# Kernel tuning notes

Hardware: AMD Instinct MI355X
Metric: run time of the kernel (lower is better)

## Reference

```python
import jax, jax.numpy as jnp
import numpy as np


def _lstm_cell(x_t, h, c, w_ih, w_hh, b):
    # x_t, h, c: [B, 1]; w_ih, w_hh: [4, 1]; b: [4]
    # PyTorch gate order: input, forget, cell(g), output
    gates = x_t @ w_ih.T + h @ w_hh.T + b  # [B, 4]
    i, f, g, o = jnp.split(gates, 4, axis=-1)
    i = jax.nn.sigmoid(i)
    f = jax.nn.sigmoid(f)
    o = jax.nn.sigmoid(o)
    g = jnp.tanh(g)
    c = f * c + i * g
    h = o * jnp.tanh(c)
    return h, c


def setup_inputs() -> dict:
    key = jax.random.key(0)
    ks = jax.random.split(key, 8)
    B, T_IN, STEPS = 32768, 1024, 512
    return {
        "x": jax.random.normal(ks[0], (B, 1, T_IN), dtype=jnp.float32),
        "t": jax.random.normal(ks[1], (B, 1, STEPS), dtype=jnp.float32),
        "h0": jax.random.normal(ks[2], (B, 1), dtype=jnp.float32),
        "c0": jax.random.normal(ks[3], (B, 1), dtype=jnp.float32),
        "w_ih": jax.random.normal(ks[4], (4, 1), dtype=jnp.float32),
        "w_hh": jax.random.normal(ks[5], (4, 1), dtype=jnp.float32),
        "b_ih": jax.random.normal(ks[6], (4,), dtype=jnp.float32) * 0.1,
        "b_hh": jax.random.normal(ks[7], (4,), dtype=jnp.float32) * 0.1,
    }


def reference(x, t, h0, c0, w_ih, w_hh, b_ih, b_hh):
    b = b_ih + b_hh
    # open loop: feed every input timestep through the LSTM cell
    xs = jnp.transpose(x[:, 0, :], (1, 0))[:, :, None]  # [T_in, B, 1]

    def open_step(carry, x_t):
        h, c = carry
        h, c = _lstm_cell(x_t, h, c, w_ih, w_hh, b)
        return (h, c), None

    (h, c), _ = jax.lax.scan(open_step, (h0, c0), xs)

    ts = jnp.transpose(t[:, 0, :], (1, 0))[:, :, None]  # [steps, B, 1]

    def closed_step(carry, _):
        h, c, x_in = carry
        h, c = _lstm_cell(x_in, h, c, w_ih, w_hh, b)
        return (h, c, h), h

    steps = ts.shape[0]
    _, preds = jax.lax.scan(closed_step, (h, c, xs[-1]), None, length=steps)
    # criterion = MSELoss(mean), accumulated per step:
    # sum_t mean_B((pred_t - t_t)^2)
    loss = jnp.sum(jnp.mean((preds - ts) ** 2, axis=(1, 2)))
    # pred_seq is detached numpy in the original -> stop_gradient here
    pred_seq = jax.lax.stop_gradient(jnp.transpose(preds[:, :, 0], (1, 0)))  # [B, steps]
    return loss, pred_seq
```

## Files before the change

### kernel.cpp

```cpp
#include <hip/hip_runtime.h>


#define L2E 1.44269504088896340736f
#define B_TOT 32768
#define T_IN 1024
#define STEPS 512
#define CH 64
#define PAD 65

__device__ __forceinline__ float ex2(float x){ return __builtin_amdgcn_exp2f(x); }
__device__ __forceinline__ float rcp(float x){ return __builtin_amdgcn_rcpf(x); }

struct K8 { float Ai,Bi,Ci, Af,Bf,Cf, Ag,Bg,Cg, Ao,Bo,Co; };
struct K4 { float Wi,Ci, Wf,Cf, Wg,Cg, Wo,Co; };

__device__ __forceinline__ void step_open(float xv, float& h, float& c, const K8& K){
    float zi = fmaf(h, K.Bi, fmaf(xv, K.Ai, K.Ci));
    float zf = fmaf(h, K.Bf, fmaf(xv, K.Af, K.Cf));
    float zg = fmaf(h, K.Bg, fmaf(xv, K.Ag, K.Cg));
    float zo = fmaf(h, K.Bo, fmaf(xv, K.Ao, K.Co));
    float ri = rcp(1.0f + ex2(zi));
    float rf = rcp(1.0f + ex2(zf));
    float rg = rcp(1.0f + ex2(zg));
    float ro = rcp(1.0f + ex2(zo));
    float g  = fmaf(-2.0f, rg, 1.0f);
    c = fmaf(rf, c, ri * g);
    float rc = rcp(1.0f + ex2((2.0f * L2E) * c));
    h = ro * fmaf(-2.0f, rc, 1.0f);
}

__device__ __forceinline__ void step_closed(float& h, float& c, const K4& K){
    float zi = fmaf(h, K.Wi, K.Ci);
    float zf = fmaf(h, K.Wf, K.Cf);
    float zg = fmaf(h, K.Wg, K.Cg);
    float zo = fmaf(h, K.Wo, K.Co);
    float ri = rcp(1.0f + ex2(zi));
    float rf = rcp(1.0f + ex2(zf));
    float rg = rcp(1.0f + ex2(zg));
    float ro = rcp(1.0f + ex2(zo));
    float g  = fmaf(-2.0f, rg, 1.0f);
    c = fmaf(rf, c, ri * g);
    float rc = rcp(1.0f + ex2((2.0f * L2E) * c));
    h = ro * fmaf(-2.0f, rc, 1.0f);
}

__device__ __forceinline__ void stage_issue(const float* __restrict__ base,
                                            int row_stride, int col0, int lane,
                                            float4* v){
    const int r_lo = lane >> 4;
    const int c4   = lane & 15;
    #pragma unroll
    for (int j = 0; j < 16; ++j){
        int r = j * 4 + r_lo;
        v[j] = *(const float4*)(base + (size_t)r * row_stride + col0 + c4 * 4);
    }
}
__device__ __forceinline__ void stage_write(float* __restrict__ lds, int lane,
                                            const float4* v){
    const int r_lo = lane >> 4;
    const int c4   = lane & 15;
    #pragma unroll
    for (int j = 0; j < 16; ++j){
        int r = j * 4 + r_lo;
        float* p = lds + r * PAD + c4 * 4;
        p[0] = v[j].x; p[1] = v[j].y; p[2] = v[j].z; p[3] = v[j].w;
    }
}

__global__ __launch_bounds__(64) void lstm_chain_kernel(
    const float* __restrict__ x, const float* __restrict__ t,
    const float* __restrict__ h0, const float* __restrict__ c0,
    const float* __restrict__ w_ih, const float* __restrict__ w_hh,
    const float* __restrict__ b_ih, const float* __restrict__ b_hh,
    float* __restrict__ out)
{
    __shared__ float sb[2][64 * PAD];
    __shared__ float pb[64 * PAD];

    const int lane = threadIdx.x;
    const int b0 = blockIdx.x * 64;
    const int b = b0 + lane;

    K8 K; K4 K2;
    {
        float bi = b_ih[0] + b_hh[0], bf = b_ih[1] + b_hh[1];
        float bg = b_ih[2] + b_hh[2], bo = b_ih[3] + b_hh[3];
        K.Ai = -L2E * w_ih[0]; K.Bi = -L2E * w_hh[0]; K.Ci = -L2E * bi;
        K.Af = -L2E * w_ih[1]; K.Bf = -L2E * w_hh[1]; K.Cf = -L2E * bf;
        K.Ag =  2.0f * L2E * w_ih[2]; K.Bg = 2.0f * L2E * w_hh[2]; K.Cg = 2.0f * L2E * bg;
        K.Ao = -L2E * w_ih[3]; K.Bo = -L2E * w_hh[3]; K.Co = -L2E * bo;
        K2.Wi = K.Ai + K.Bi; K2.Ci = K.Ci;
        K2.Wf = K.Af + K.Bf; K2.Cf = K.Cf;
        K2.Wg = K.Ag + K.Bg; K2.Cg = K.Cg;
        K2.Wo = K.Ao + K.Bo; K2.Co = K.Co;
    }

    float h = h0[b];
    float c = c0[b];

    const float* xbase = x + (size_t)b0 * T_IN;
    const float* tbase = t + (size_t)b0 * STEPS;

    {
        float4 stg[16];
        stage_issue(xbase, T_IN, 0, lane, stg);
        stage_write(sb[0], lane, stg);
    }
    #pragma unroll 1
    for (int k = 0; k < T_IN / CH; ++k){
        float4 stg2[16];
        if (k < T_IN / CH - 1) stage_issue(xbase, T_IN, (k + 1) * CH, lane, stg2);
        const float* xrow = &sb[k & 1][lane * PAD];
        #pragma unroll 4
        for (int s = 0; s < CH; ++s){
            step_open(xrow[s], h, c, K);
        }
        if (k < T_IN / CH - 1) stage_write(sb[(k + 1) & 1], lane, stg2);
    }
    float xin = sb[(T_IN / CH - 1) & 1][lane * PAD + (CH - 1)];

    {
        float4 stg[16];
        stage_issue(tbase, STEPS, 0, lane, stg);
        stage_write(sb[0], lane, stg);
    }
    float lacc = 0.0f;
    #pragma unroll 1
    for (int k = 0; k < STEPS / CH; ++k){
        float4 stg2[16];
        if (k < STEPS / CH - 1) stage_issue(tbase, STEPS, (k + 1) * CH, lane, stg2);
        const float* trow = &sb[k & 1][lane * PAD];
        float* prow = &pb[lane * PAD];
        #pragma unroll 4
        for (int s = 0; s < CH; ++s){
            if (k == 0 && s == 0) step_open(xin, h, c, K);
            else                  step_closed(h, c, K2);
            float d = h - trow[s];
            lacc = fmaf(d, d, lacc);
            prow[s] = h;
        }
        float* obase = out + 1 + (size_t)b0 * STEPS + k * CH + lane;
        #pragma unroll 4
        for (int r = 0; r < 64; ++r){
            obase[(size_t)r * STEPS] = pb[r * PAD + lane];
        }
        if (k < STEPS / CH - 1) stage_write(sb[(k + 1) & 1], lane, stg2);
    }

    #pragma unroll
    for (int off = 32; off > 0; off >>= 1)
        lacc += __shfl_down(lacc, off, 64);
    if (lane == 0)
        atomicAdd(out, lacc * (1.0f / (float)B_TOT));
}

extern "C" void kernel_launch(void* const* d_in, const int* in_sizes, int n_in,
                              void* d_out, int out_size, void* d_ws, size_t ws_size,
                              hipStream_t stream) {
    const float* x    = (const float*)d_in[0];
    const float* t    = (const float*)d_in[1];
    const float* h0   = (const float*)d_in[2];
    const float* c0   = (const float*)d_in[3];
    const float* w_ih = (const float*)d_in[4];
    const float* w_hh = (const float*)d_in[5];
    const float* b_ih = (const float*)d_in[6];
    const float* b_hh = (const float*)d_in[7];
    float* out = (float*)d_out;

    hipMemsetAsync(out, 0, sizeof(float), stream);

    lstm_chain_kernel<<<B_TOT / 64, 64, 0, stream>>>(
        x, t, h0, c0, w_ih, w_hh, b_ih, b_hh, out);
}
```

Measured before the change: 355.4 us.

## Split each LSTM chain across two lanes with DPP gate exchange

Each batch element's recurrence is now handled by a lane pair: one lane computes input/cell gates, the other forget/output, exchanging sigmoid results via DPP quad permute. Blocks cover 32 chains instead of 64, doubling the wave count to fill more SIMDs and shortening the per-step transcendental chain per lane. The cell state is kept prescaled to fold a multiply, and the loss is halved to account for duplicated lanes. Costs include redundant cell/tanh work in both lanes and extra DPP/select instructions.

New measurement: 331.1 us. 6.8% less time.

```diff
diff --git a/kernel.cpp b/kernel.cpp
--- a/kernel.cpp
+++ b/kernel.cpp
@@ -5,65 +5,53 @@
 #define B_TOT 32768
 #define T_IN 1024
 #define STEPS 512
+#define CPB 32
 #define CH 64
 #define PAD 65
 
 __device__ __forceinline__ float ex2(float x){ return __builtin_amdgcn_exp2f(x); }
 __device__ __forceinline__ float rcp(float x){ return __builtin_amdgcn_rcpf(x); }
-
-struct K8 { float Ai,Bi,Ci, Af,Bf,Cf, Ag,Bg,Cg, Ao,Bo,Co; };
-struct K4 { float Wi,Ci, Wf,Cf, Wg,Cg, Wo,Co; };
-
-__device__ __forceinline__ void step_open(float xv, float& h, float& c, const K8& K){
-    float zi = fmaf(h, K.Bi, fmaf(xv, K.Ai, K.Ci));
-    float zf = fmaf(h, K.Bf, fmaf(xv, K.Af, K.Cf));
-    float zg = fmaf(h, K.Bg, fmaf(xv, K.Ag, K.Cg));
-    float zo = fmaf(h, K.Bo, fmaf(xv, K.Ao, K.Co));
-    float ri = rcp(1.0f + ex2(zi));
-    float rf = rcp(1.0f + ex2(zf));
-    float rg = rcp(1.0f + ex2(zg));
-    float ro = rcp(1.0f + ex2(zo));
-    float g  = fmaf(-2.0f, rg, 1.0f);
-    c = fmaf(rf, c, ri * g);
-    float rc = rcp(1.0f + ex2((2.0f * L2E) * c));
-    h = ro * fmaf(-2.0f, rc, 1.0f);
+__device__ __forceinline__ float dpp_swap1(float v){
+    return __int_as_float(__builtin_amdgcn_mov_dpp(__float_as_int(v), 0xB1, 0xF, 0xF, true));
 }
 
-__device__ __forceinline__ void step_closed(float& h, float& c, const K4& K){
-    float zi = fmaf(h, K.Wi, K.Ci);
-    float zf = fmaf(h, K.Wf, K.Cf);
-    float zg = fmaf(h, K.Wg, K.Cg);
-    float zo = fmaf(h, K.Wo, K.Co);
-    float ri = rcp(1.0f + ex2(zi));
-    float rf = rcp(1.0f + ex2(zf));
-    float rg = rcp(1.0f + ex2(zg));
-    float ro = rcp(1.0f + ex2(zo));
-    float g  = fmaf(-2.0f, rg, 1.0f);
-    c = fmaf(rf, c, ri * g);
-    float rc = rcp(1.0f + ex2((2.0f * L2E) * c));
-    h = ro * fmaf(-2.0f, rc, 1.0f);
+struct LaneK { float A1,B1,C1, A2,B2,C2, W1,W2; };
+
+__device__ __forceinline__ void finish_step(float z1, float z2, bool odd,
+                                            float& h, float& C){
+    float e1 = ex2(z1);
+    float e2 = ex2(z2);
+    float r1 = rcp(1.0f + e1);
+    float r2 = rcp(1.0f + e2);
+    float s1 = dpp_swap1(r1);
+    float s2 = dpp_swap1(r2);
+    float ri = odd ? s1 : r1;
+    float rf = odd ? r1 : s1;
+    float rg = odd ? s2 : r2;
+    float ro = odd ? r2 : s2;
+    float g2  = fmaf(rg, -4.0f * L2E, 2.0f * L2E);
+    float rfC = rf * C;
+    C = fmaf(ri, g2, rfC);
+    float rc = rcp(1.0f + ex2(C));
+    float u  = rc + rc;
+    h = fmaf(-u, ro, ro);
 }
 
-__device__ __forceinline__ void stage_issue(const float* __restrict__ base,
-                                            int row_stride, int col0, int lane,
-                                            float4* v){
-    const int r_lo = lane >> 4;
-    const int c4   = lane & 15;
+__device__ __forceinline__ void stage_issue32(const float* __restrict__ base,
+                                              int row_stride, int col0, int lane,
+                                              float4* v){
+    const int r_lo = lane >> 4, c4 = lane & 15;
     #pragma unroll
-    for (int j = 0; j < 16; ++j){
-        int r = j * 4 + r_lo;
-        v[j] = *(const float4*)(base + (size_t)r * row_stride + col0 + c4 * 4);
-    }
+    for (int j = 0; j < 8; ++j)
+        v[j] = *(const float4*)(base + (size_t)(j*4 + r_lo) * row_stride + col0 + c4*4);
 }
-__device__ __forceinline__ void stage_write(float* __restrict__ lds, int lane,
-                                            const float4* v){
-    const int r_lo = lane >> 4;
-    const int c4   = lane & 15;
+__device__ __forceinline__ void stage_write32(float* __restrict__ lds, int lane,
+                                              const float4* v){
+    const int r_lo = lane >> 4, c4 = lane & 15;
     #pragma unroll
-    for (int j = 0; j < 16; ++j){
-        int r = j * 4 + r_lo;
-        float* p = lds + r * PAD + c4 * 4;
-        p[0] = v[j].x; p[1] = v[j].y; p[2] = v[j].z; p[3] = v[j].w;
+    for (int j = 0; j < 8; ++j){
+        float* p = lds + (j*4 + r_lo) * PAD + c4*4;
+        p[0]=v[j].x; p[1]=v[j].y; p[2]=v[j].z; p[3]=v[j].w;
     }
 }
 
@@ -74,84 +62,93 @@
     const float* __restrict__ b_ih, const float* __restrict__ b_hh,
     float* __restrict__ out)
 {
-    __shared__ float sb[2][64 * PAD];
-    __shared__ float pb[64 * PAD];
+    __shared__ float sb[2][CPB * PAD];
+    __shared__ float pb[CPB * PAD];
 
     const int lane = threadIdx.x;
-    const int b0 = blockIdx.x * 64;
-    const int b = b0 + lane;
+    const bool odd = lane & 1;
+    const int ch   = lane >> 1;
+    const int b0   = blockIdx.x * CPB;
 
-    K8 K; K4 K2;
+    LaneK K;
     {
         float bi = b_ih[0] + b_hh[0], bf = b_ih[1] + b_hh[1];
         float bg = b_ih[2] + b_hh[2], bo = b_ih[3] + b_hh[3];
-        K.Ai = -L2E * w_ih[0]; K.Bi = -L2E * w_hh[0]; K.Ci = -L2E * bi;
-        K.Af = -L2E * w_ih[1]; K.Bf = -L2E * w_hh[1]; K.Cf = -L2E * bf;
-        K.Ag =  2.0f * L2E * w_ih[2]; K.Bg = 2.0f * L2E * w_hh[2]; K.Cg = 2.0f * L2E * bg;
-        K.Ao = -L2E * w_ih[3]; K.Bo = -L2E * w_hh[3]; K.Co = -L2E * bo;
-        K2.Wi = K.Ai + K.Bi; K2.Ci = K.Ci;
-        K2.Wf = K.Af + K.Bf; K2.Cf = K.Cf;
-        K2.Wg = K.Ag + K.Bg; K2.Cg = K.Cg;
-        K2.Wo = K.Ao + K.Bo; K2.Co = K.Co;
+        float Ai = -L2E*w_ih[0], Bi = -L2E*w_hh[0], Ci = -L2E*bi;
+        float Af = -L2E*w_ih[1], Bf = -L2E*w_hh[1], Cf = -L2E*bf;
+        float Ag = 2.0f*L2E*w_ih[2], Bg = 2.0f*L2E*w_hh[2], Cg = 2.0f*L2E*bg;
+        float Ao = -L2E*w_ih[3], Bo = -L2E*w_hh[3], Co = -L2E*bo;
+        K.A1 = odd ? Af : Ai;  K.B1 = odd ? Bf : Bi;  K.C1 = odd ? Cf : Ci;
+        K.A2 = odd ? Ao : Ag;  K.B2 = odd ? Bo : Bg;  K.C2 = odd ? Co : Cg;
+        K.W1 = K.A1 + K.B1;    K.W2 = K.A2 + K.B2;
     }
 
-    float h = h0[b];
-    float c = c0[b];
+    float h = h0[b0 + ch];
+    float C = (2.0f * L2E) * c0[b0 + ch];
 
     const float* xbase = x + (size_t)b0 * T_IN;
     const float* tbase = t + (size_t)b0 * STEPS;
 
-    {
-        float4 stg[16];
-        stage_issue(xbase, T_IN, 0, lane, stg);
-        stage_write(sb[0], lane, stg);
-    }
+    { float4 stg[8]; stage_issue32(xbase, T_IN, 0, lane, stg); stage_write32(sb[0], lane, stg); }
     #pragma unroll 1
     for (int k = 0; k < T_IN / CH; ++k){
-        float4 stg2[16];
-        if (k < T_IN / CH - 1) stage_issue(xbase, T_IN, (k + 1) * CH, lane, stg2);
-        const float* xrow = &sb[k & 1][lane * PAD];
+        float4 stg[8];
+        if (k < T_IN/CH - 1) stage_issue32(xbase, T_IN, (k+1)*CH, lane, stg);
+        const float* xrow = &sb[k & 1][ch * PAD];
         #pragma unroll 4
         for (int s = 0; s < CH; ++s){
-            step_open(xrow[s], h, c, K);
+            float xv = xrow[s];
+            float z1 = fmaf(xv, K.A1, fmaf(h, K.B1, K.C1));
+            float z2 = fmaf(xv, K.A2, fmaf(h, K.B2, K.C2));
+            finish_step(z1, z2, odd, h, C);
         }
-        if (k < T_IN / CH - 1) stage_write(sb[(k + 1) & 1], lane, stg2);
+        if (k < T_IN/CH - 1) stage_write32(sb[(k+1) & 1], lane, stg);
     }
-    float xin = sb[(T_IN / CH - 1) & 1][lane * PAD + (CH - 1)];
+    float xin = sb[(T_IN/CH - 1) & 1][ch * PAD + (CH - 1)];
 
-    {
-        float4 stg[16];
-        stage_issue(tbase, STEPS, 0, lane, stg);
-        stage_write(sb[0], lane, stg);
-    }
+    { float4 stg[8]; stage_issue32(tbase, STEPS, 0, lane, stg); stage_write32(sb[0], lane, stg); }
     float lacc = 0.0f;
+
+    auto cstep = [&](int s, const float* trow, float* prow){
+        float z1 = fmaf(h, K.W1, K.C1);
+        float z2 = fmaf(h, K.W2, K.C2);
+        finish_step(z1, z2, odd, h, C);
+        float d = h - trow[s];
+        lacc = fmaf(d, d, lacc);
+        prow[s] = h;
+    };
+
     #pragma unroll 1
     for (int k = 0; k < STEPS / CH; ++k){
-        float4 stg2[16];
-        if (k < STEPS / CH - 1) stage_issue(tbase, STEPS, (k + 1) * CH, lane, stg2);
-        const float* trow = &sb[k & 1][lane * PAD];
-        float* prow = &pb[lane * PAD];
+        float4 stg[8];
+        if (k < STEPS/CH - 1) stage_issue32(tbase, STEPS, (k+1)*CH, lane, stg);
+        const float* trow = &sb[k & 1][ch * PAD];
+        float* prow = &pb[ch * PAD];
+        if (k == 0){
+            float z1 = fmaf(xin, K.A1, fmaf(h, K.B1, K.C1));
+            float z2 = fmaf(xin, K.A2, fmaf(h, K.B2, K.C2));
+            finish_step(z1, z2, odd, h, C);
+            float d = h - trow[0];
+            lacc = fmaf(d, d, lacc);
+            prow[0] = h;
+            #pragma unroll 4
+            for (int s = 1; s < CH; ++s) cstep(s, trow, prow);
+        } else {
+            #pragma unroll 4
+            for (int s = 0; s < CH; ++s) cstep(s, trow, prow);
+        }
+        float* obase = out + 1 + (size_t)b0 * STEPS + k * CH;
         #pragma unroll 4
-        for (int s = 0; s < CH; ++s){
-            if (k == 0 && s == 0) step_open(xin, h, c, K);
-            else                  step_closed(h, c, K2);
-            float d = h - trow[s];
-            lacc = fmaf(d, d, lacc);
-            prow[s] = h;
-        }
-        float* obase = out + 1 + (size_t)b0 * STEPS + k * CH + lane;
-        #pragma unroll 4
-        for (int r = 0; r < 64; ++r){
-            obase[(size_t)r * STEPS] = pb[r * PAD + lane];
-        }
-        if (k < STEPS / CH - 1) stage_write(sb[(k + 1) & 1], lane, stg2);
+        for (int r = 0; r < CPB; ++r)
+            obase[(size_t)r * STEPS + lane] = pb[r * PAD + lane];
+        if (k < STEPS/CH - 1) stage_write32(sb[(k+1) & 1], lane, stg);
     }
 
     #pragma unroll
     for (int off = 32; off > 0; off >>= 1)
         lacc += __shfl_down(lacc, off, 64);
     if (lane == 0)
-        atomicAdd(out, lacc * (1.0f / (float)B_TOT));
+        atomicAdd(out, lacc * (0.5f / (float)B_TOT));
 }
 
 extern "C" void kernel_launch(void* const* d_in, const int* in_sizes, int n_in,
@@ -169,6 +166,6 @@
 
     hipMemsetAsync(out, 0, sizeof(float), stream);
 
-    lstm_chain_kernel<<<B_TOT / 64, 64, 0, stream>>>(
+    lstm_chain_kernel<<<B_TOT / CPB, 64, 0, stream>>>(
         x, t, h0, c0, w_ih, w_hh, b_ih, b_hh, out);
 }
```
